# Kernel tuning notes

Hardware: AMD Instinct MI355X
Metric: run time of the kernel (lower is better)

The kernel has to match this reference:

```python
import jax, jax.numpy as jnp
import numpy as np

MAX_WAVELENGTH = 10000.0
NUM_HEADS = 15
NUM_KV_HEADS = 5
HEAD_DIM = 64


def apply_rope(x, positions):
    """RoPE: x [B, L, H, D], positions [B, L] (int)."""
    d_half = x.shape[-1] // 2
    x = x.astype(jnp.float32)
    freq_exponents = (2.0 / x.shape[-1]) * jnp.arange(d_half, dtype=jnp.float32)
    timescale = MAX_WAVELENGTH ** freq_exponents  # [d_half]
    radians = positions[..., None].astype(jnp.float32) / timescale  # [B, L, d_half]
    radians = radians[..., None, :]  # [B, L, 1, d_half]
    sin, cos = jnp.sin(radians), jnp.cos(radians)
    x1, x2 = x[..., :d_half], x[..., d_half:]
    return jnp.concatenate([x1 * cos - x2 * sin, x2 * cos + x1 * sin], axis=-1)


def setup_inputs() -> dict:
    key = jax.random.key(0)
    k1, k2, k3, k4 = jax.random.split(key, 4)
    B, L = 2, 2048
    query_states = jax.random.normal(k1, (B, L, NUM_HEADS, HEAD_DIM), dtype=jnp.float32)
    key_states = jax.random.normal(k2, (B, L, NUM_KV_HEADS, HEAD_DIM), dtype=jnp.float32)
    value_states = jax.random.normal(k3, (B, L, NUM_KV_HEADS, HEAD_DIM), dtype=jnp.float32)
    positions = jnp.sort(jax.random.randint(k4, (B, L), 0, L, dtype=jnp.int32), axis=-1)
    # Causal (prefix-LM) boolean mask [B, L, L]
    attention_mask = jnp.broadcast_to(jnp.tril(jnp.ones((L, L), dtype=bool)), (B, L, L))
    return {
        "query_states": query_states,
        "key_states": key_states,
        "value_states": value_states,
        "positions": positions,
        "attention_mask": attention_mask,
    }


def reference(query_states, key_states, value_states, positions, attention_mask):
    B, L = query_states.shape[0], query_states.shape[1]
    groups = NUM_HEADS // NUM_KV_HEADS  # 3

    # RoPE on Q and K (eager, per original module)
    q = apply_rope(query_states, positions)  # [B, L, 15, 64] fp32
    k = apply_rope(key_states, positions)    # [B, L, 5, 64]  fp32

    # GQA expansion: [B, L, Kv, D] -> [B, L, Kv*groups, D]
    k = jnp.repeat(k, groups, axis=2)
    v = jnp.repeat(value_states, groups, axis=2).astype(jnp.float32)

    # Scores in fp32: [B, H, Lq, Lk]
    scores = jnp.einsum("bqhd,bkhd->bhqk", q, k) * (HEAD_DIM ** -0.5)
    big_neg = jnp.finfo(jnp.float32).min
    scores = jnp.where(attention_mask[:, None, :, :], scores, big_neg)
    probs = jax.nn.softmax(scores, axis=-1)

    out = jnp.einsum("bhqk,bkhd->bqhd", probs, v)  # [B, L, H, D]
    return out.reshape(B, L, NUM_HEADS * HEAD_DIM)  # [B, L, 960]
```

## Files before the change

kernel.cpp:

```cpp
#include <hip/hip_runtime.h>
#include <math.h>

#define NB 2
#define NL 2048
#define NHQ 15
#define NKV 5
#define HD 64
#define NT 32
#define GRP 3
#define PST 72
#define NG 16
#define SLOTF 2080

typedef __attribute__((ext_vector_type(8))) short short8;
typedef __attribute__((ext_vector_type(4))) float floatx4;

#define ROPE_C 0.28782313662425575f
#define QSCALE 0.18033688011116016f

__device__ __forceinline__ ushort f2bf(float x) {
    unsigned u = __builtin_bit_cast(unsigned, x);
    u = (u + 0x7FFFu + ((u >> 16) & 1u)) >> 16;
    return (ushort)u;
}
__device__ __forceinline__ unsigned pk2(float a, float b) {
    unsigned ua = __builtin_bit_cast(unsigned, a) + 0x8000u;
    unsigned ub = __builtin_bit_cast(unsigned, b) + 0x8000u;
    return __builtin_amdgcn_perm(ub, ua, 0x07060302u);
}
__device__ __forceinline__ void async16(ushort* lds, const ushort* g) {
    __builtin_amdgcn_global_load_lds(
        (const __attribute__((address_space(1))) unsigned int*)g,
        (__attribute__((address_space(3))) unsigned int*)lds, 16, 0, 0);
}

union U8  { short8 v; ushort u[8]; };
union F8  { float4 f4[2]; float f[8]; };

__global__ __launch_bounds__(256)
void prep_kv(const float* __restrict__ K, const float* __restrict__ V,
             const int* __restrict__ pos, ushort* __restrict__ Kr,
             ushort* __restrict__ Vr) {
    __shared__ float Vs[64][65];
    const int bid = blockIdx.x, t = threadIdx.x;
    if (bid < NB * NKV * NT) {
        int b = bid / (NKV * NT), rem = bid % (NKV * NT);
        int h = rem / NT, k0 = (rem % NT) * 64;
        int j = t >> 2, c0 = t & 3;
        int row = k0 + j;
        const float* src = K + ((size_t)((b * NL + row) * NKV + h)) * HD;
        int db = c0 * 8;
        F8 x1, x2;
        x1.f4[0] = *(const float4*)&src[db];
        x1.f4[1] = *(const float4*)&src[db + 4];
        x2.f4[0] = *(const float4*)&src[db + 32];
        x2.f4[1] = *(const float4*)&src[db + 36];
        float ps = (float)pos[b * NL + row];
        U8 lo, hi;
#pragma unroll
        for (int i = 0; i < 8; ++i) {
            float inv = __expf((float)(db + i) * -ROPE_C);
            float sn, cs; __sincosf(ps * inv, &sn, &cs);
            lo.u[i] = f2bf(x1.f[i] * cs - x2.f[i] * sn);
            hi.u[i] = f2bf(x2.f[i] * cs + x1.f[i] * sn);
        }
        ushort* dst = Kr + (size_t)bid * 4096;
        *(short8*)&dst[(j * 8 + (c0 ^ (j & 7))) * 8]       = lo.v;
        *(short8*)&dst[(j * 8 + ((c0 + 4) ^ (j & 7))) * 8] = hi.v;
    } else {
        int vb = bid - NB * NKV * NT;
        int b = vb / (NKV * NT), rem = vb % (NKV * NT);
        int h = rem / NT, k0 = (rem % NT) * 64;
#pragma unroll
        for (int it = 0; it < 4; ++it) {
            int e = t + it * 256;
            int j = e >> 4, d4 = (e & 15) * 4;
            *(float4*)&Vs[j][d4] =
                *(const float4*)&V[((size_t)((b * NL + k0 + j) * NKV + h)) * HD + d4];
        }
        __syncthreads();
        ushort* dst = Vr + (size_t)vb * 4096;
#pragma unroll
        for (int it = 0; it < 2; ++it) {
            int o = t + it * 256;
            int d = o >> 3, c = o & 7, j0 = c * 8;
            U8 r;
#pragma unroll
            for (int k = 0; k < 8; ++k) r.u[k] = f2bf(Vs[j0 + k][d]);
            *(short8*)&dst[(d * 8 + (c ^ (d & 7))) * 8] = r.v;
        }
    }
}

__global__ __launch_bounds__(256, 4)
void attn_partial(const float* __restrict__ Q, const ushort* __restrict__ Kr,
                  const ushort* __restrict__ Vr, const int* __restrict__ pos,
                  float* __restrict__ Pw, float* __restrict__ out,
                  int CH, int TOT) {
    __shared__ __align__(16) ushort Kb[2][4096];
    __shared__ __align__(16) ushort Vb[2][4096];
    __shared__ __align__(16) ushort Pb[4][2][16 * PST];

    const int t = threadIdx.x;
    const int w = t >> 6, lane = t & 63;
    const int l16 = lane & 15, quad = lane >> 4;
    const int h = blockIdx.y, b = blockIdx.z;
    const int kvh = h / GRP;
    const int fidx = TOT - 1 - (int)blockIdx.x;

    int g = 0, chunk = fidx;
    for (; g < NG; ++g) {
        int nc = (2 * g + 2 + CH - 1) / CH;
        if (chunk < nc) break;
        chunk -= nc;
    }
    const int ntg = 2 * g + 2;
    const int nc  = (ntg + CH - 1) / CH;
    const int kb0 = chunk * CH;
    int kb1 = kb0 + CH; if (kb1 > ntg) kb1 = ntg;
    const int qi = 4 * g + w;
    const int ntw = (qi >> 1) + 1;
    const int r0 = qi * 32;

    short8 Qa[2][2];
#pragma unroll
    for (int rf = 0; rf < 2; ++rf) {
        int row = r0 + rf * 16 + l16;
        const float* src = Q + ((size_t)((b * NL + row) * NHQ + h)) * HD;
        int db = quad * 8;
        F8 x1, x2;
        x1.f4[0] = *(const float4*)&src[db];
        x1.f4[1] = *(const float4*)&src[db + 4];
        x2.f4[0] = *(const float4*)&src[db + 32];
        x2.f4[1] = *(const float4*)&src[db + 36];
        float ps = (float)pos[b * NL + row];
        union { short8 v; unsigned u[4]; } lo, hi;
#pragma unroll
        for (int i = 0; i < 8; i += 2) {
            float inv0 = __expf((float)(db + i) * -ROPE_C);
            float inv1 = __expf((float)(db + i + 1) * -ROPE_C);
            float sn0, cs0, sn1, cs1;
            __sincosf(ps * inv0, &sn0, &cs0);
            __sincosf(ps * inv1, &sn1, &cs1);
            float l0 = (x1.f[i] * cs0 - x2.f[i] * sn0) * QSCALE;
            float l1 = (x1.f[i + 1] * cs1 - x2.f[i + 1] * sn1) * QSCALE;
            float h0 = (x2.f[i] * cs0 + x1.f[i] * sn0) * QSCALE;
            float h1 = (x2.f[i + 1] * cs1 + x1.f[i + 1] * sn1) * QSCALE;
            lo.u[i >> 1] = pk2(l0, l1);
            hi.u[i >> 1] = pk2(h0, h1);
        }
        Qa[rf][0] = lo.v;
        Qa[rf][1] = hi.v;
    }

    floatx4 O[2][4];
    float lsum[2] = {0.f, 0.f};
#pragma unroll
    for (int rf = 0; rf < 2; ++rf)
#pragma unroll
        for (int d = 0; d < 4; ++d) O[rf][d] = (floatx4){0.f, 0.f, 0.f, 0.f};

    const ushort* Kt0 = Kr + (size_t)((b * NKV + kvh) * NT) * 4096;
    const ushort* Vt0 = Vr + (size_t)((b * NKV + kvh) * NT) * 4096;
    const int swz8[2] = { ((quad)     ^ (l16 & 7)) * 8,
                          ((quad + 4) ^ (l16 & 7)) * 8 };
    const int so = w * 1024;

    {
        const ushort* Kt = Kt0 + (size_t)kb0 * 4096;
        const ushort* Vt = Vt0 + (size_t)kb0 * 4096;
        async16(&Kb[0][so],       Kt + so + lane * 8);
        async16(&Kb[0][so + 512], Kt + so + 512 + lane * 8);
        async16(&Vb[0][so],       Vt + so + lane * 8);
        async16(&Vb[0][so + 512], Vt + so + 512 + lane * 8);
    }
    __syncthreads();

    int p = 0;
    for (int kb = kb0; kb < kb1; ++kb, p ^= 1) {
        if (kb + 1 < kb1) {
            const ushort* Kt = Kt0 + (size_t)(kb + 1) * 4096;
            const ushort* Vt = Vt0 + (size_t)(kb + 1) * 4096;
            async16(&Kb[p ^ 1][so],       Kt + so + lane * 8);
            async16(&Kb[p ^ 1][so + 512], Kt + so + 512 + lane * 8);
            async16(&Vb[p ^ 1][so],       Vt + so + lane * 8);
            async16(&Vb[p ^ 1][so + 512], Vt + so + 512 + lane * 8);
        }

        if (kb < ntw) {
            floatx4 S[2][4];
#pragma unroll
            for (int rf = 0; rf < 2; ++rf)
#pragma unroll
                for (int c = 0; c < 4; ++c) S[rf][c] = (floatx4){0.f, 0.f, 0.f, 0.f};
#pragma unroll
            for (int s = 0; s < 2; ++s)
#pragma unroll
                for (int c = 0; c < 4; ++c) {
                    short8 kfv = *(const short8*)&Kb[p][(c * 16 + l16) * 64 + swz8[s]];
                    S[0][c] = __builtin_amdgcn_mfma_f32_16x16x32_bf16(kfv, Qa[0][s], S[0][c], 0, 0, 0);
                    S[1][c] = __builtin_amdgcn_mfma_f32_16x16x32_bf16(kfv, Qa[1][s], S[1][c], 0, 0, 0);
                }

            const bool diag = (kb == ntw - 1);
#pragma unroll
            for (int rf = 0; rf < 2; ++rf) {
                int qrow = r0 + rf * 16 + l16;
                float acc = 0.f;
#pragma unroll
                for (int c = 0; c < 4; ++c) {
                    float pv[4];
#pragma unroll
                    for (int r = 0; r < 4; ++r) {
                        int key = kb * 64 + c * 16 + quad * 4 + r;
                        float sv = S[rf][c][r];
                        if (diag && key > qrow) sv = -1e30f;
                        pv[r] = exp2f(sv);
                        acc += pv[r];
                    }
                    *(uint2*)&Pb[w][rf][l16 * PST + c * 16 + quad * 4] =
                        make_uint2(pk2(pv[0], pv[1]), pk2(pv[2], pv[3]));
                }
                lsum[rf] += acc;
            }

#pragma unroll
            for (int s = 0; s < 2; ++s) {
                short8 pf0 = *(const short8*)&Pb[w][0][l16 * PST + s * 32 + quad * 8];
                short8 pf1 = *(const short8*)&Pb[w][1][l16 * PST + s * 32 + quad * 8];
#pragma unroll
                for (int d = 0; d < 4; ++d) {
                    short8 vfv = *(const short8*)&Vb[p][(d * 16 + l16) * 64 + swz8[s]];
                    O[0][d] = __builtin_amdgcn_mfma_f32_16x16x32_bf16(vfv, pf0, O[0][d], 0, 0, 0);
                    O[1][d] = __builtin_amdgcn_mfma_f32_16x16x32_bf16(vfv, pf1, O[1][d], 0, 0, 0);
                }
            }
        }
        __syncthreads();
    }

    if (nc == 1) {
#pragma unroll
        for (int rf = 0; rf < 2; ++rf) {
            float ls = lsum[rf];
            ls += __shfl_xor(ls, 16, 64);
            ls += __shfl_xor(ls, 32, 64);
            float rinv = 1.0f / ls;
            int qrow = r0 + rf * 16 + l16;
            float* op = out + (size_t)(b * NL + qrow) * (NHQ * HD) + h * HD;
#pragma unroll
            for (int d = 0; d < 4; ++d) {
                float4 o = make_float4(O[rf][d][0] * rinv, O[rf][d][1] * rinv,
                                       O[rf][d][2] * rinv, O[rf][d][3] * rinv);
                *(float4*)&op[d * 16 + quad * 4] = o;
            }
        }
    } else {
        float* slot = Pw + (((size_t)(b * NHQ + h) * TOT + fidx) * 4 + w) * SLOTF;
#pragma unroll
        for (int rf = 0; rf < 2; ++rf) {
#pragma unroll
            for (int d = 0; d < 4; ++d) {
                float4 o = make_float4(O[rf][d][0], O[rf][d][1], O[rf][d][2], O[rf][d][3]);
                *(float4*)&slot[(rf * 16 + l16) * 64 + d * 16 + quad * 4] = o;
            }
            float ls = lsum[rf];
            ls += __shfl_xor(ls, 16, 64);
            ls += __shfl_xor(ls, 32, 64);
            if (quad == 0) slot[2048 + rf * 16 + l16] = ls;
        }
    }
}

__global__ __launch_bounds__(256)
void combine(const float* __restrict__ Pw, float* __restrict__ out,
             int CH, int TOT, int qi0) {
    __shared__ float ls[32];
    const int qi = qi0 + blockIdx.x;
    const int bh = blockIdx.y;
    const int b = bh / NHQ, h = bh % NHQ;
    const int g = qi >> 2, w = qi & 3;
    const int nch = (2 * g + 2 + CH - 1) / CH;
    int pfx = 0;
    for (int gg = 0; gg < g; ++gg) pfx += (2 * gg + 2 + CH - 1) / CH;
    const float* base = Pw + (((size_t)bh * TOT + pfx) * 4 + w) * SLOTF;

    const int t = threadIdx.x;
    const int rl = t >> 3, d0 = (t & 7) * 8;
    float a[8];
#pragma unroll
    for (int k = 0; k < 8; ++k) a[k] = 0.f;
    float lacc = 0.f;
    for (int c = 0; c < nch; ++c) {
        const float* pb = base + (size_t)c * 4 * SLOTF;
        float4 x0 = *(const float4*)&pb[rl * 64 + d0];
        float4 x1 = *(const float4*)&pb[rl * 64 + d0 + 4];
        a[0] += x0.x; a[1] += x0.y; a[2] += x0.z; a[3] += x0.w;
        a[4] += x1.x; a[5] += x1.y; a[6] += x1.z; a[7] += x1.w;
        if (t < 32) lacc += pb[2048 + t];
    }
    if (t < 32) ls[t] = lacc;
    __syncthreads();
    float rinv = 1.0f / ls[rl];
    float* op = out + (size_t)(b * NL + qi * 32 + rl) * (NHQ * HD) + h * HD + d0;
    *(float4*)&op[0] = make_float4(a[0] * rinv, a[1] * rinv, a[2] * rinv, a[3] * rinv);
    *(float4*)&op[4] = make_float4(a[4] * rinv, a[5] * rinv, a[6] * rinv, a[7] * rinv);
}

extern "C" void kernel_launch(void* const* d_in, const int* in_sizes, int n_in,
                              void* d_out, int out_size, void* d_ws, size_t ws_size,
                              hipStream_t stream) {
    const float* Q   = (const float*)d_in[0];
    const float* K   = (const float*)d_in[1];
    const float* V   = (const float*)d_in[2];
    const int*   pos = (const int*)d_in[3];
    ushort* Kr = (ushort*)d_ws;
    ushort* Vr = Kr + (size_t)NB * NKV * NT * 4096;
    float*  Pw = (float*)(Vr + (size_t)NB * NKV * NT * 4096);
    float*  out = (float*)d_out;
    const size_t prepBytes = (size_t)2 * NB * NKV * NT * 4096 * sizeof(ushort);

    int CH = 32, TOT = NG;
    const int ladder[2] = {8, 16};
    for (int i = 0; i < 2; ++i) {
        int ch = ladder[i], tot = 0;
        for (int gq = 0; gq < NG; ++gq) tot += (2 * gq + 2 + ch - 1) / ch;
        size_t need = prepBytes + (size_t)NB * NHQ * tot * 4 * SLOTF * sizeof(float);
        if (need <= ws_size) { CH = ch; TOT = tot; break; }
    }

    prep_kv<<<2 * NB * NKV * NT, 256, 0, stream>>>(K, V, pos, Kr, Vr);
    dim3 grid(TOT, NHQ, NB);
    attn_partial<<<grid, 256, 0, stream>>>(Q, Kr, Vr, pos, Pw, out, CH, TOT);
    int qi0 = 2 * CH;
    if (qi0 < 64)
        combine<<<dim3(64 - qi0, NB * NHQ), 256, 0, stream>>>(Pw, out, CH, TOT, qi0);
}
```

Baseline: 154.2 us.

## Single-buffer K/V tiles, split diagonal masking branch, try smaller KV chunk size

Removes double buffering of K/V tiles in shared memory, so each iteration loads its tile and synchronizes before compute. This halves the K/V LDS footprint, which could allow more resident blocks, but gives up overlap of the next tile's load with compute. The causal mask check is moved into a separate branch so non-diagonal tiles skip per-element comparisons. The chunk ladder now tries CH=4 first, producing more split-K blocks and more combine work in exchange for better load balance.

```diff
diff --git a/kernel.cpp b/kernel.cpp
--- a/kernel.cpp
+++ b/kernel.cpp
@@ -97,8 +97,8 @@
                   const ushort* __restrict__ Vr, const int* __restrict__ pos,
                   float* __restrict__ Pw, float* __restrict__ out,
                   int CH, int TOT) {
-    __shared__ __align__(16) ushort Kb[2][4096];
-    __shared__ __align__(16) ushort Vb[2][4096];
+    __shared__ __align__(16) ushort Kb[4096];
+    __shared__ __align__(16) ushort Vb[4096];
     __shared__ __align__(16) ushort Pb[4][2][16 * PST];
 
     const int t = threadIdx.x;
@@ -110,9 +110,9 @@
 
     int g = 0, chunk = fidx;
     for (; g < NG; ++g) {
-        int nc = (2 * g + 2 + CH - 1) / CH;
-        if (chunk < nc) break;
-        chunk -= nc;
+        int ncg = (2 * g + 2 + CH - 1) / CH;
+        if (chunk < ncg) break;
+        chunk -= ncg;
     }
     const int ntg = 2 * g + 2;
     const int nc  = (ntg + CH - 1) / CH;
@@ -166,26 +166,16 @@
                           ((quad + 4) ^ (l16 & 7)) * 8 };
     const int so = w * 1024;
 
-    {
-        const ushort* Kt = Kt0 + (size_t)kb0 * 4096;
-        const ushort* Vt = Vt0 + (size_t)kb0 * 4096;
-        async16(&Kb[0][so],       Kt + so + lane * 8);
-        async16(&Kb[0][so + 512], Kt + so + 512 + lane * 8);
-        async16(&Vb[0][so],       Vt + so + lane * 8);
-        async16(&Vb[0][so + 512], Vt + so + 512 + lane * 8);
-    }
-    __syncthreads();
-
-    int p = 0;
-    for (int kb = kb0; kb < kb1; ++kb, p ^= 1) {
-        if (kb + 1 < kb1) {
-            const ushort* Kt = Kt0 + (size_t)(kb + 1) * 4096;
-            const ushort* Vt = Vt0 + (size_t)(kb + 1) * 4096;
-            async16(&Kb[p ^ 1][so],       Kt + so + lane * 8);
-            async16(&Kb[p ^ 1][so + 512], Kt + so + 512 + lane * 8);
-            async16(&Vb[p ^ 1][so],       Vt + so + lane * 8);
-            async16(&Vb[p ^ 1][so + 512], Vt + so + 512 + lane * 8);
-        }
+    for (int kb = kb0; kb < kb1; ++kb) {
+        {
+            const ushort* Kt = Kt0 + (size_t)kb * 4096;
+            const ushort* Vt = Vt0 + (size_t)kb * 4096;
+            async16(&Kb[so],       Kt + so + lane * 8);
+            async16(&Kb[so + 512], Kt + so + 512 + lane * 8);
+            async16(&Vb[so],       Vt + so + lane * 8);
+            async16(&Vb[so + 512], Vt + so + 512 + lane * 8);
+        }
+        __syncthreads();
 
         if (kb < ntw) {
             floatx4 S[2][4];
@@ -197,31 +187,49 @@
             for (int s = 0; s < 2; ++s)
 #pragma unroll
                 for (int c = 0; c < 4; ++c) {
-                    short8 kfv = *(const short8*)&Kb[p][(c * 16 + l16) * 64 + swz8[s]];
+                    short8 kfv = *(const short8*)&Kb[(c * 16 + l16) * 64 + swz8[s]];
                     S[0][c] = __builtin_amdgcn_mfma_f32_16x16x32_bf16(kfv, Qa[0][s], S[0][c], 0, 0, 0);
                     S[1][c] = __builtin_amdgcn_mfma_f32_16x16x32_bf16(kfv, Qa[1][s], S[1][c], 0, 0, 0);
                 }
 
-            const bool diag = (kb == ntw - 1);
-#pragma unroll
-            for (int rf = 0; rf < 2; ++rf) {
-                int qrow = r0 + rf * 16 + l16;
-                float acc = 0.f;
-#pragma unroll
-                for (int c = 0; c < 4; ++c) {
-                    float pv[4];
-#pragma unroll
-                    for (int r = 0; r < 4; ++r) {
-                        int key = kb * 64 + c * 16 + quad * 4 + r;
-                        float sv = S[rf][c][r];
-                        if (diag && key > qrow) sv = -1e30f;
-                        pv[r] = exp2f(sv);
-                        acc += pv[r];
+            if (kb == ntw - 1) {
+#pragma unroll
+                for (int rf = 0; rf < 2; ++rf) {
+                    int qrow = r0 + rf * 16 + l16;
+                    float acc = 0.f;
+#pragma unroll
+                    for (int c = 0; c < 4; ++c) {
+                        float pv[4];
+#pragma unroll
+                        for (int r = 0; r < 4; ++r) {
+                            int key = kb * 64 + c * 16 + quad * 4 + r;
+                            float sv = S[rf][c][r];
+                            if (key > qrow) sv = -1e30f;
+                            pv[r] = exp2f(sv);
+                            acc += pv[r];
+                        }
+                        *(uint2*)&Pb[w][rf][l16 * PST + c * 16 + quad * 4] =
+                            make_uint2(pk2(pv[0], pv[1]), pk2(pv[2], pv[3]));
                     }
-                    *(uint2*)&Pb[w][rf][l16 * PST + c * 16 + quad * 4] =
-                        make_uint2(pk2(pv[0], pv[1]), pk2(pv[2], pv[3]));
+                    lsum[rf] += acc;
                 }
-                lsum[rf] += acc;
+            } else {
+#pragma unroll
+                for (int rf = 0; rf < 2; ++rf) {
+                    float acc = 0.f;
+#pragma unroll
+                    for (int c = 0; c < 4; ++c) {
+                        float pv[4];
+#pragma unroll
+                        for (int r = 0; r < 4; ++r) {
+                            pv[r] = exp2f(S[rf][c][r]);
+                            acc += pv[r];
+                        }
+                        *(uint2*)&Pb[w][rf][l16 * PST + c * 16 + quad * 4] =
+                            make_uint2(pk2(pv[0], pv[1]), pk2(pv[2], pv[3]));
+                    }
+                    lsum[rf] += acc;
+                }
             }
 
 #pragma unroll
@@ -230,7 +238,7 @@
                 short8 pf1 = *(const short8*)&Pb[w][1][l16 * PST + s * 32 + quad * 8];
 #pragma unroll
                 for (int d = 0; d < 4; ++d) {
-                    short8 vfv = *(const short8*)&Vb[p][(d * 16 + l16) * 64 + swz8[s]];
+                    short8 vfv = *(const short8*)&Vb[(d * 16 + l16) * 64 + swz8[s]];
                     O[0][d] = __builtin_amdgcn_mfma_f32_16x16x32_bf16(vfv, pf0, O[0][d], 0, 0, 0);
                     O[1][d] = __builtin_amdgcn_mfma_f32_16x16x32_bf16(vfv, pf1, O[1][d], 0, 0, 0);
                 }
@@ -321,8 +329,8 @@
     const size_t prepBytes = (size_t)2 * NB * NKV * NT * 4096 * sizeof(ushort);
 
     int CH = 32, TOT = NG;
-    const int ladder[2] = {8, 16};
-    for (int i = 0; i < 2; ++i) {
+    const int ladder[3] = {4, 8, 16};
+    for (int i = 0; i < 3; ++i) {
         int ch = ladder[i], tot = 0;
         for (int gq = 0; gq < NG; ++gq) tot += (2 * gq + 2 + ch - 1) / ch;
         size_t need = prepBytes + (size_t)NB * NHQ * tot * 4 * SLOTF * sizeof(float);
```

After: 150.8 us. -2.2%, faster.
